# Optimization experiments

Hardware: AMD Instinct MI355X
Metric: run time of the kernel (lower is better)

Reference implementation:

```python
import jax, jax.numpy as jnp
import numpy as np

N, E, G = 100000, 300000, 4096
F_IN, ED, A = 32, 4, 80

def _glorot(k, shape):
    return jax.random.normal(k, shape, dtype=jnp.float32) / np.sqrt(shape[0])

def setup_inputs() -> dict:
    key = jax.random.key(0)
    ks = jax.random.split(key, 24)
    src = jax.random.randint(ks[0], (E,), 0, N, dtype=jnp.int32)
    # guarantee no self loops so PyG's remove_self_loops is a no-op
    dst = ((src + jax.random.randint(ks[1], (E,), 1, N, dtype=jnp.int32)) % N).astype(jnp.int32)
    return dict(
        x=jax.random.normal(ks[2], (N, F_IN), jnp.float32),
        edge_index=jnp.stack([src, dst]),
        edge_attr=jax.random.uniform(ks[3], (E, ED), jnp.float32),
        batch=jnp.sort(jax.random.randint(ks[4], (N,), 0, G, dtype=jnp.int32)),
        action_mask=jnp.ones((G, A), dtype=bool),
        num_graphs=G,
        gin_We=_glorot(ks[5], (ED, F_IN)), gin_be=jnp.zeros((F_IN,), jnp.float32),
        gin_W1=_glorot(ks[6], (F_IN, 64)), gin_b1=jnp.zeros((64,), jnp.float32),
        gin_W2=_glorot(ks[7], (64, 64)), gin_b2=jnp.zeros((64,), jnp.float32),
        g2_Wl=_glorot(ks[8], (64, 256)), g2_bl=jnp.zeros((256,), jnp.float32),
        g2_Wr=_glorot(ks[9], (64, 256)), g2_br=jnp.zeros((256,), jnp.float32),
        g2_We=_glorot(ks[10], (ED, 256)),
        g2_att=jax.random.normal(ks[11], (4, 64), jnp.float32) / np.sqrt(64.0),
        g2_bias=jnp.zeros((256,), jnp.float32),
        g3_Wl=_glorot(ks[12], (256, 256)), g3_bl=jnp.zeros((256,), jnp.float32),
        g3_Wr=_glorot(ks[13], (256, 256)), g3_br=jnp.zeros((256,), jnp.float32),
        g3_We=_glorot(ks[14], (ED, 256)),
        g3_att=jax.random.normal(ks[15], (2, 128), jnp.float32) / np.sqrt(128.0),
        g3_bias=jnp.zeros((128,), jnp.float32),
        pool_W=_glorot(ks[16], (128, 1)), pool_b=jnp.zeros((1,), jnp.float32),
        act_W1=_glorot(ks[17], (128, 64)), act_b1=jnp.zeros((64,), jnp.float32),
        act_W2=_glorot(ks[18], (64, A)), act_b2=jnp.zeros((A,), jnp.float32),
        cr_W1=_glorot(ks[19], (128, 64)), cr_b1=jnp.zeros((64,), jnp.float32),
        cr_W2=_glorot(ks[20], (64, 1)), cr_b2=jnp.zeros((1,), jnp.float32),
    )

def _seg_softmax(s, seg, n):
    # s: [E, H]; softmax over entries sharing seg id (every target has a self loop)
    m = jax.ops.segment_max(s, seg, num_segments=n)
    ex = jnp.exp(s - m[seg])
    z = jax.ops.segment_sum(ex, seg, num_segments=n)
    return ex / z[seg]

def _gatv2(x, src, dst, ea, Wl, bl, Wr, br, We, att, bias, heads, ch, concat, n):
    xl = (x @ Wl + bl).reshape(n, heads, ch)   # message side (x_j)
    xr = (x @ Wr + br).reshape(n, heads, ch)   # target side (x_i)
    e = jax.nn.leaky_relu(xl[src] + xr[dst] + (ea @ We).reshape(-1, heads, ch), 0.2)
    score = jnp.einsum('ehc,hc->eh', e, att)   # [E, H]
    alpha = _seg_softmax(score, dst, n)
    out = jax.ops.segment_sum(xl[src] * alpha[..., None], dst, num_segments=n)
    out = out.reshape(n, heads * ch) if concat else out.mean(axis=1)
    return out + bias

def reference(x, edge_index, edge_attr, batch, action_mask, num_graphs,
              gin_We, gin_be, gin_W1, gin_b1, gin_W2, gin_b2,
              g2_Wl, g2_bl, g2_Wr, g2_br, g2_We, g2_att, g2_bias,
              g3_Wl, g3_bl, g3_Wr, g3_br, g3_We, g3_att, g3_bias,
              pool_W, pool_b, act_W1, act_b1, act_W2, act_b2,
              cr_W1, cr_b1, cr_W2, cr_b2):
    n = x.shape[0]
    src, dst = edge_index[0], edge_index[1]
    # --- GINEConv (eps=0): nn(x + sum_j relu(x_j + lin(e_ij))) ---
    m = jax.nn.relu(x[src] + edge_attr @ gin_We + gin_be)
    h = x + jax.ops.segment_sum(m, dst, num_segments=n)
    h = jax.nn.relu(h @ gin_W1 + gin_b1) @ gin_W2 + gin_b2
    x1 = jax.nn.relu(h)
    # --- self loops with fill_value='mean' edge_attr (shared by both GATv2 layers) ---
    s = jax.ops.segment_sum(edge_attr, dst, num_segments=n)
    cnt = jax.ops.segment_sum(jnp.ones((dst.shape[0],), edge_attr.dtype), dst, num_segments=n)
    loop_attr = s / jnp.maximum(cnt, 1.0)[:, None]
    ar = jnp.arange(n, dtype=src.dtype)
    src2 = jnp.concatenate([src, ar])
    dst2 = jnp.concatenate([dst, ar])
    ea2 = jnp.concatenate([edge_attr, loop_attr], axis=0)
    # --- GATv2 layers ---
    x2 = jax.nn.relu(_gatv2(x1, src2, dst2, ea2, g2_Wl, g2_bl, g2_Wr, g2_br, g2_We, g2_att, g2_bias, 4, 64, True, n))
    x3 = jax.nn.relu(_gatv2(x2, src2, dst2, ea2, g3_Wl, g3_bl, g3_Wr, g3_br, g3_We, g3_att, g3_bias, 2, 128, False, n))
    # --- AttentionalAggregation: softmax(sigmoid(gate), batch) weighted sum ---
    gate = jax.nn.sigmoid(x3 @ pool_W + pool_b)[:, 0]
    alpha = _seg_softmax(gate[:, None], batch, num_graphs)
    emb = jax.ops.segment_sum(alpha * x3, batch, num_segments=num_graphs)
    # --- heads ---
    logits = jax.nn.relu(emb @ act_W1 + act_b1) @ act_W2 + act_b2
    val = jax.nn.relu(emb @ cr_W1 + cr_b1) @ cr_W2 + cr_b2
    logits = jnp.where(action_mask, logits, jnp.finfo(logits.dtype).min)
    return logits, val
```

## Files before the change

### kernel.cpp

```cpp
#include <hip/hip_runtime.h>
#include <math.h>

#define NN 100000
#define NE 300000
#define NG 4096
#define NA 80
#define NB_SCAN 391

typedef __attribute__((ext_vector_type(8))) short short8;
typedef __attribute__((ext_vector_type(4))) float f32x4;

__device__ __forceinline__ float bf2f(unsigned short h){
  return __uint_as_float(((unsigned)h)<<16);
}
__device__ __forceinline__ unsigned short f2bf(float f){
  unsigned u = __float_as_uint(f);
  unsigned r = u + 0x7FFFu + ((u>>16)&1u);
  return (unsigned short)(r>>16);
}
__device__ __forceinline__ void ld_bf4(const unsigned short* p, float o[4]){
  uint2 u = *(const uint2*)p;
  o[0] = __uint_as_float(u.x<<16);
  o[1] = __uint_as_float(u.x & 0xffff0000u);
  o[2] = __uint_as_float(u.y<<16);
  o[3] = __uint_as_float(u.y & 0xffff0000u);
}

__device__ __forceinline__ unsigned fenc(float f){
  unsigned u = __float_as_uint(f);
  return (u & 0x80000000u) ? ~u : (u | 0x80000000u);
}
__device__ __forceinline__ float fdec(unsigned u){
  return (u & 0x80000000u) ? __uint_as_float(u & 0x7fffffffu) : __uint_as_float(~u);
}
#define ENC_NEG_INF 0x007FFFFFu

__global__ __launch_bounds__(256) void fill_u32(unsigned* p, unsigned v, int n){
  int i = blockIdx.x*256 + threadIdx.x;
  if (i < n) p[i] = v;
}

__global__ __launch_bounds__(256) void deg_count(const int* __restrict__ dst, int* __restrict__ deg){
  int e = blockIdx.x*256 + threadIdx.x;
  if (e < NE) atomicAdd(&deg[dst[e]], 1);
}

__global__ __launch_bounds__(256) void scan1(const int* __restrict__ deg, int* __restrict__ row_ptr, int* __restrict__ bsum){
  __shared__ int sh[256];
  int t = threadIdx.x, g = blockIdx.x*256 + t;
  int v = (g < NN) ? deg[g] : 0;
  sh[t] = v;
  __syncthreads();
  for (int off=1; off<256; off<<=1){
    int xv = (t>=off) ? sh[t-off] : 0;
    __syncthreads();
    sh[t] += xv;
    __syncthreads();
  }
  if (g < NN) row_ptr[g] = sh[t] - v;
  if (t == 255) bsum[blockIdx.x] = sh[t];
}

__global__ __launch_bounds__(512) void scan2(int* __restrict__ bsum){
  __shared__ int sh[512];
  int t = threadIdx.x;
  int v = (t < NB_SCAN) ? bsum[t] : 0;
  sh[t] = v;
  __syncthreads();
  for (int off=1; off<512; off<<=1){
    int xv = (t>=off) ? sh[t-off] : 0;
    __syncthreads();
    sh[t] += xv;
    __syncthreads();
  }
  if (t < NB_SCAN) bsum[t] = sh[t] - v;
}

__global__ __launch_bounds__(256) void scan3(int* __restrict__ row_ptr, const int* __restrict__ bsum, int* __restrict__ cursor){
  int g = blockIdx.x*256 + threadIdx.x;
  if (g < NN){
    int r = row_ptr[g] + bsum[g>>8];
    row_ptr[g] = r;
    cursor[g] = r;
  }
}

__global__ __launch_bounds__(256) void scatter_edges(
    const int* __restrict__ dst, const int* __restrict__ src, const float4* __restrict__ ea4,
    int* __restrict__ cursor, int* __restrict__ srcs, float4* __restrict__ eas){
  int e = blockIdx.x*256 + threadIdx.x;
  if (e < NE){
    int pos = atomicAdd(&cursor[dst[e]], 1);
    srcs[pos] = src[e];
    eas[pos]  = ea4[e];
  }
}

__global__ __launch_bounds__(256) void gine_gather(
    const float* __restrict__ x, const int* __restrict__ srcs,
    const int* __restrict__ row_ptr, const int* __restrict__ deg,
    const float4* __restrict__ eas, const float* __restrict__ We, const float* __restrict__ be,
    float* __restrict__ hacc, float* __restrict__ lattr){
  int ch = threadIdx.x & 31, ln = threadIdx.x >> 5;
  int nd = blockIdx.x*8 + ln;
  if (nd >= NN) return;
  int rs = row_ptr[nd], d = deg[nd];
  float accv = 0.f, asum = 0.f;
  float bev = be[ch];
  float w0=We[ch], w1=We[32+ch], w2=We[64+ch], w3=We[96+ch];
  for (int j=0;j<d;++j){
    int s = srcs[rs+j];
    float4 a = eas[rs+j];
    float m = x[s*32+ch] + a.x*w0 + a.y*w1 + a.z*w2 + a.w*w3 + bev;
    accv += (m>0.f)? m : 0.f;
    if (ch < 4) asum += (ch==0)?a.x:(ch==1)?a.y:(ch==2)?a.z:a.w;
  }
  hacc[nd*32+ch] = accv;
  if (ch < 4) lattr[nd*4+ch] = asum / (float)(d>0? d:1);
}

__global__ __launch_bounds__(256) void wt_prep2(
    const float* __restrict__ W, unsigned short* __restrict__ H,
    unsigned short* __restrict__ L, int K, int N){
  int k = blockIdx.x;
  int n = threadIdx.x;
  if (n >= N) return;
  float v = W[k*N + n];
  unsigned short h = f2bf(v);
  unsigned short l = f2bf(v - bf2f(h));
  H[n*K + k] = h;
  L[n*K + k] = l;
}

__global__ __launch_bounds__(512) void gine_mlp_mfma(
    const float* __restrict__ x, const float* __restrict__ hacc,
    const unsigned short* __restrict__ W1h, const unsigned short* __restrict__ W1l,
    const float* __restrict__ b1,
    const unsigned short* __restrict__ W2h, const unsigned short* __restrict__ W2l,
    const float* __restrict__ b2,
    unsigned short* __restrict__ x1b){
  __shared__ unsigned short hS[256*36];
  __shared__ unsigned short t1S[256*68];
  int t = threadIdx.x;
  int row0 = blockIdx.x*256;
  const float4* x4 = (const float4*)x;
  const float4* h4 = (const float4*)hacc;
  #pragma unroll
  for (int j=0;j<4;++j){
    int i = t + j*512;
    int row = i>>3, cq = i&7;
    int grow = row0 + row;
    float4 xv = {0,0,0,0}, hv = {0,0,0,0};
    if (grow < NN){ xv = x4[(size_t)grow*8 + cq]; hv = h4[(size_t)grow*8 + cq]; }
    uint2 o;
    o.x = (unsigned)f2bf(xv.x+hv.x) | ((unsigned)f2bf(xv.y+hv.y)<<16);
    o.y = (unsigned)f2bf(xv.z+hv.z) | ((unsigned)f2bf(xv.w+hv.w)<<16);
    *(uint2*)&hS[row*36 + cq*4] = o;
  }
  int w = t>>6, l = t&63, lr = l&15, lk = l>>4;
  short8 w1h[4], w1l[4];
  #pragma unroll
  for (int nt=0;nt<4;++nt){
    int n = nt*16 + lr;
    w1h[nt] = *(const short8*)(W1h + n*32 + lk*8);
    w1l[nt] = *(const short8*)(W1l + n*32 + lk*8);
  }
  __syncthreads();
  int rw = w*32;
  {
    short8 a0 = *(const short8*)&hS[(rw+lr)*36 + lk*8];
    short8 a1 = *(const short8*)&hS[(rw+16+lr)*36 + lk*8];
    f32x4 acc0[4], acc1[4];
    #pragma unroll
    for (int nt=0;nt<4;++nt){ acc0[nt]=(f32x4){0,0,0,0}; acc1[nt]=(f32x4){0,0,0,0}; }
    #pragma unroll
    for (int nt=0;nt<4;++nt){
      acc0[nt] = __builtin_amdgcn_mfma_f32_16x16x32_bf16(a0, w1h[nt], acc0[nt], 0,0,0);
      acc0[nt] = __builtin_amdgcn_mfma_f32_16x16x32_bf16(a0, w1l[nt], acc0[nt], 0,0,0);
      acc1[nt] = __builtin_amdgcn_mfma_f32_16x16x32_bf16(a1, w1h[nt], acc1[nt], 0,0,0);
      acc1[nt] = __builtin_amdgcn_mfma_f32_16x16x32_bf16(a1, w1l[nt], acc1[nt], 0,0,0);
    }
    #pragma unroll
    for (int nt=0;nt<4;++nt){
      int col = nt*16 + lr;
      float bv = b1[col];
      #pragma unroll
      for (int j=0;j<4;++j){
        int r = rw + lk*4 + j;
        float v0 = acc0[nt][j] + bv; v0 = (v0>0.f)?v0:0.f;
        float v1 = acc1[nt][j] + bv; v1 = (v1>0.f)?v1:0.f;
        t1S[r*68 + col]      = f2bf(v0);
        t1S[(r+16)*68 + col] = f2bf(v1);
      }
    }
  }
  short8 w2h[4][2], w2l[4][2];
  #pragma unroll
  for (int nt=0;nt<4;++nt){
    int n = nt*16 + lr;
    #pragma unroll
    for (int kc=0;kc<2;++kc){
      w2h[nt][kc] = *(const short8*)(W2h + n*64 + kc*32 + lk*8);
      w2l[nt][kc] = *(const short8*)(W2l + n*64 + kc*32 + lk*8);
    }
  }
  __syncthreads();
  {
    f32x4 acc0[4], acc1[4];
    #pragma unroll
    for (int nt=0;nt<4;++nt){ acc0[nt]=(f32x4){0,0,0,0}; acc1[nt]=(f32x4){0,0,0,0}; }
    #pragma unroll
    for (int kc=0;kc<2;++kc){
      short8 a0 = *(const short8*)&t1S[(rw+lr)*68 + kc*32 + lk*8];
      short8 a1 = *(const short8*)&t1S[(rw+16+lr)*68 + kc*32 + lk*8];
      #pragma unroll
      for (int nt=0;nt<4;++nt){
        acc0[nt] = __builtin_amdgcn_mfma_f32_16x16x32_bf16(a0, w2h[nt][kc], acc0[nt], 0,0,0);
        acc0[nt] = __builtin_amdgcn_mfma_f32_16x16x32_bf16(a0, w2l[nt][kc], acc0[nt], 0,0,0);
        acc1[nt] = __builtin_amdgcn_mfma_f32_16x16x32_bf16(a1, w2h[nt][kc], acc1[nt], 0,0,0);
        acc1[nt] = __builtin_amdgcn_mfma_f32_16x16x32_bf16(a1, w2l[nt][kc], acc1[nt], 0,0,0);
      }
    }
    #pragma unroll
    for (int nt=0;nt<4;++nt){
      int col = nt*16 + lr;
      float bv = b2[col];
      #pragma unroll
      for (int j=0;j<4;++j){
        int r0 = row0 + rw + lk*4 + j;
        int r1 = r0 + 16;
        float v0 = acc0[nt][j] + bv; v0 = (v0>0.f)?v0:0.f;
        float v1 = acc1[nt][j] + bv; v1 = (v1>0.f)?v1:0.f;
        if (r0 < NN) x1b[(size_t)r0*64 + col] = f2bf(v0);
        if (r1 < NN) x1b[(size_t)r1*64 + col] = f2bf(v1);
      }
    }
  }
}

template<int KIN>
__global__ __launch_bounds__(512) void mfma_lin(
    const unsigned short* __restrict__ Abf,
    const unsigned short* __restrict__ Wth,
    const unsigned short* __restrict__ Wtl,
    const float* __restrict__ bias,
    unsigned short* __restrict__ Yout){
  __shared__ unsigned short WhS[256*40];
  __shared__ unsigned short WlS[256*40];
  int t = threadIdx.x, w = t>>6, l = t&63;
  int lr = l & 15, lk = l >> 4;
  int row0 = blockIdx.x*256 + w*32;
  f32x4 acc0[16], acc1[16];
  #pragma unroll
  for (int i=0;i<16;++i){ acc0[i] = (f32x4){0,0,0,0}; acc1[i] = (f32x4){0,0,0,0}; }
  int ar0 = row0 + lr;      if (ar0 > NN-1) ar0 = NN-1;
  int ar1 = row0 + 16 + lr; if (ar1 > NN-1) ar1 = NN-1;
  const unsigned short* Ab0 = Abf + (size_t)ar0*KIN + lk*8;
  const unsigned short* Ab1 = Abf + (size_t)ar1*KIN + lk*8;
  const int sn = t>>1, sh16 = (t&1)*16;
  const unsigned short* Wh_g = Wth + (size_t)sn*KIN + sh16;
  const unsigned short* Wl_g = Wtl + (size_t)sn*KIN + sh16;

  short8 ph0, ph1, pl0, pl1;
  ph0 = *(const short8*)(Wh_g);     ph1 = *(const short8*)(Wh_g + 8);
  pl0 = *(const short8*)(Wl_g);     pl1 = *(const short8*)(Wl_g + 8);

  constexpr int NKC = KIN/32;
  for (int kc=0; kc<NKC; ++kc){
    *(short8*)&WhS[sn*40 + sh16]     = ph0;
    *(short8*)&WhS[sn*40 + sh16 + 8] = ph1;
    *(short8*)&WlS[sn*40 + sh16]     = pl0;
    *(short8*)&WlS[sn*40 + sh16 + 8] = pl1;
    __syncthreads();
    if (kc+1 < NKC){
      ph0 = *(const short8*)(Wh_g + (kc+1)*32);
      ph1 = *(const short8*)(Wh_g + (kc+1)*32 + 8);
      pl0 = *(const short8*)(Wl_g + (kc+1)*32);
      pl1 = *(const short8*)(Wl_g + (kc+1)*32 + 8);
    }
    short8 a0 = *(const short8*)(Ab0 + kc*32);
    short8 a1 = *(const short8*)(Ab1 + kc*32);
    #pragma unroll
    for (int nt=0; nt<16; ++nt){
      int n = nt*16 + lr;
      short8 bh = *(const short8*)&WhS[n*40 + lk*8];
      short8 bl = *(const short8*)&WlS[n*40 + lk*8];
      acc0[nt] = __builtin_amdgcn_mfma_f32_16x16x32_bf16(a0, bh, acc0[nt], 0,0,0);
      acc0[nt] = __builtin_amdgcn_mfma_f32_16x16x32_bf16(a0, bl, acc0[nt], 0,0,0);
      acc1[nt] = __builtin_amdgcn_mfma_f32_16x16x32_bf16(a1, bh, acc1[nt], 0,0,0);
      acc1[nt] = __builtin_amdgcn_mfma_f32_16x16x32_bf16(a1, bl, acc1[nt], 0,0,0);
    }
    __syncthreads();
  }

  #pragma unroll
  for (int nt=0; nt<16; ++nt){
    int col = nt*16 + lr;
    float bv = bias[col];
    #pragma unroll
    for (int j=0;j<4;++j){
      int r0 = row0 + lk*4 + j;
      int r1 = r0 + 16;
      if (r0 < NN) Yout[(size_t)r0*256 + col] = f2bf(acc0[nt][j] + bv);
      if (r1 < NN) Yout[(size_t)r1*256 + col] = f2bf(acc1[nt][j] + bv);
    }
  }
}

__global__ __launch_bounds__(256) void gat_fused4(
    const int* __restrict__ srcs, const int* __restrict__ row_ptr,
    const int* __restrict__ deg, const float4* __restrict__ eas,
    const float* __restrict__ lattr,
    const unsigned short* __restrict__ xlb, const unsigned short* __restrict__ xrb,
    const float* __restrict__ We, const float* __restrict__ att,
    const float* __restrict__ bias, unsigned short* __restrict__ x2b){
  int t = threadIdx.x;
  int lane = t & 63, w = t >> 6;
  int nd = blockIdx.x*4 + w;
  if (nd >= NN) return;
  const int c0 = lane*4;
  float4 w0 = *(const float4*)(We + c0);
  float4 w1 = *(const float4*)(We + 256 + c0);
  float4 w2 = *(const float4*)(We + 512 + c0);
  float4 w3 = *(const float4*)(We + 768 + c0);
  float4 at = *(const float4*)(att + c0);
  float4 bs = *(const float4*)(bias + c0);
  float xrv[4]; ld_bf4(xrb + (size_t)nd*256 + c0, xrv);
  float4 la = *(const float4*)(lattr + (size_t)nd*4);
  int rs = row_ptr[nd], d = deg[nd];

  float acc0,acc1,acc2,acc3, m, l;
  {
    float xlv[4]; ld_bf4(xlb + (size_t)nd*256 + c0, xlv);
    float pv, v;
    v = xlv[0]+xrv[0] + la.x*w0.x+la.y*w1.x+la.z*w2.x+la.w*w3.x; v=(v>0.f)?v:0.2f*v; pv  = v*at.x;
    v = xlv[1]+xrv[1] + la.x*w0.y+la.y*w1.y+la.z*w2.y+la.w*w3.y; v=(v>0.f)?v:0.2f*v; pv += v*at.y;
    v = xlv[2]+xrv[2] + la.x*w0.z+la.y*w1.z+la.z*w2.z+la.w*w3.z; v=(v>0.f)?v:0.2f*v; pv += v*at.z;
    v = xlv[3]+xrv[3] + la.x*w0.w+la.y*w1.w+la.z*w2.w+la.w*w3.w; v=(v>0.f)?v:0.2f*v; pv += v*at.w;
    pv += __shfl_xor(pv,1,64); pv += __shfl_xor(pv,2,64);
    pv += __shfl_xor(pv,4,64); pv += __shfl_xor(pv,8,64);
    m = pv; l = 1.f;
    acc0=xlv[0]; acc1=xlv[1]; acc2=xlv[2]; acc3=xlv[3];
  }
  for (int j=0;j<d;++j){
    int s = srcs[rs+j];
    float4 a = eas[rs+j];
    float xlv[4]; ld_bf4(xlb + (size_t)s*256 + c0, xlv);
    float pv, v;
    v = xlv[0]+xrv[0] + a.x*w0.x+a.y*w1.x+a.z*w2.x+a.w*w3.x; v=(v>0.f)?v:0.2f*v; pv  = v*at.x;
    v = xlv[1]+xrv[1] + a.x*w0.y+a.y*w1.y+a.z*w2.y+a.w*w3.y; v=(v>0.f)?v:0.2f*v; pv += v*at.y;
    v = xlv[2]+xrv[2] + a.x*w0.z+a.y*w1.z+a.z*w2.z+a.w*w3.z; v=(v>0.f)?v:0.2f*v; pv += v*at.z;
    v = xlv[3]+xrv[3] + a.x*w0.w+a.y*w1.w+a.z*w2.w+a.w*w3.w; v=(v>0.f)?v:0.2f*v; pv += v*at.w;
    pv += __shfl_xor(pv,1,64); pv += __shfl_xor(pv,2,64);
    pv += __shfl_xor(pv,4,64); pv += __shfl_xor(pv,8,64);
    float mn = fmaxf(m, pv);
    float c1 = __expf(m-mn), c2 = __expf(pv-mn);
    l = l*c1 + c2;
    acc0 = acc0*c1 + c2*xlv[0]; acc1 = acc1*c1 + c2*xlv[1];
    acc2 = acc2*c1 + c2*xlv[2]; acc3 = acc3*c1 + c2*xlv[3];
    m = mn;
  }
  float rl = 1.f/l;
  float o0 = acc0*rl + bs.x; o0 = (o0>0.f)?o0:0.f;
  float o1 = acc1*rl + bs.y; o1 = (o1>0.f)?o1:0.f;
  float o2 = acc2*rl + bs.z; o2 = (o2>0.f)?o2:0.f;
  float o3 = acc3*rl + bs.w; o3 = (o3>0.f)?o3:0.f;
  uint2 ov;
  ov.x = (unsigned)f2bf(o0) | ((unsigned)f2bf(o1)<<16);
  ov.y = (unsigned)f2bf(o2) | ((unsigned)f2bf(o3)<<16);
  *(uint2*)(x2b + (size_t)nd*256 + c0) = ov;
}

__global__ __launch_bounds__(256) void gat_fused2b(
    const int* __restrict__ srcs, const int* __restrict__ row_ptr,
    const int* __restrict__ deg, const float4* __restrict__ eas,
    const float* __restrict__ lattr,
    const unsigned short* __restrict__ xlb, const unsigned short* __restrict__ xrb,
    const float* __restrict__ We, const float* __restrict__ att,
    const float* __restrict__ bias, float* __restrict__ x3){
  int t = threadIdx.x;
  int lane = t & 63, w = t >> 6;
  int nd = blockIdx.x*4 + w;
  if (nd >= NN) return;
  const int c0 = lane*4;
  const int cm = c0 & 127;
  float4 w0 = *(const float4*)(We + c0);
  float4 w1 = *(const float4*)(We + 256 + c0);
  float4 w2 = *(const float4*)(We + 512 + c0);
  float4 w3 = *(const float4*)(We + 768 + c0);
  float4 at = *(const float4*)(att + c0);
  float4 bs = *(const float4*)(bias + cm);
  float xrv[4]; ld_bf4(xrb + (size_t)nd*256 + c0, xrv);
  float4 la = *(const float4*)(lattr + (size_t)nd*4);
  int rs = row_ptr[nd], d = deg[nd];

  float acc0,acc1,acc2,acc3, m, l;
  {
    float xlv[4]; ld_bf4(xlb + (size_t)nd*256 + c0, xlv);
    float pv, v;
    v = xlv[0]+xrv[0] + la.x*w0.x+la.y*w1.x+la.z*w2.x+la.w*w3.x; v=(v>0.f)?v:0.2f*v; pv  = v*at.x;
    v = xlv[1]+xrv[1] + la.x*w0.y+la.y*w1.y+la.z*w2.y+la.w*w3.y; v=(v>0.f)?v:0.2f*v; pv += v*at.y;
    v = xlv[2]+xrv[2] + la.x*w0.z+la.y*w1.z+la.z*w2.z+la.w*w3.z; v=(v>0.f)?v:0.2f*v; pv += v*at.z;
    v = xlv[3]+xrv[3] + la.x*w0.w+la.y*w1.w+la.z*w2.w+la.w*w3.w; v=(v>0.f)?v:0.2f*v; pv += v*at.w;
    pv += __shfl_xor(pv,1,64); pv += __shfl_xor(pv,2,64);
    pv += __shfl_xor(pv,4,64); pv += __shfl_xor(pv,8,64); pv += __shfl_xor(pv,16,64);
    m = pv; l = 1.f;
    acc0=xlv[0]; acc1=xlv[1]; acc2=xlv[2]; acc3=xlv[3];
  }
  for (int j=0;j<d;++j){
    int s = srcs[rs+j];
    float4 a = eas[rs+j];
    float xlv[4]; ld_bf4(xlb + (size_t)s*256 + c0, xlv);
    float pv, v;
    v = xlv[0]+xrv[0] + a.x*w0.x+a.y*w1.x+a.z*w2.x+a.w*w3.x; v=(v>0.f)?v:0.2f*v; pv  = v*at.x;
    v = xlv[1]+xrv[1] + a.x*w0.y+a.y*w1.y+a.z*w2.y+a.w*w3.y; v=(v>0.f)?v:0.2f*v; pv += v*at.y;
    v = xlv[2]+xrv[2] + a.x*w0.z+a.y*w1.z+a.z*w2.z+a.w*w3.z; v=(v>0.f)?v:0.2f*v; pv += v*at.z;
    v = xlv[3]+xrv[3] + a.x*w0.w+a.y*w1.w+a.z*w2.w+a.w*w3.w; v=(v>0.f)?v:0.2f*v; pv += v*at.w;
    pv += __shfl_xor(pv,1,64); pv += __shfl_xor(pv,2,64);
    pv += __shfl_xor(pv,4,64); pv += __shfl_xor(pv,8,64); pv += __shfl_xor(pv,16,64);
    float mn = fmaxf(m, pv);
    float c1 = __expf(m-mn), c2 = __expf(pv-mn);
    l = l*c1 + c2;
    acc0 = acc0*c1 + c2*xlv[0]; acc1 = acc1*c1 + c2*xlv[1];
    acc2 = acc2*c1 + c2*xlv[2]; acc3 = acc3*c1 + c2*xlv[3];
    m = mn;
  }
  float rl = 1.f/l;
  float h0 = acc0*rl, h1 = acc1*rl, h2 = acc2*rl, h3 = acc3*rl;
  float p0 = __shfl_xor(h0,32,64), p1 = __shfl_xor(h1,32,64);
  float p2 = __shfl_xor(h2,32,64), p3 = __shfl_xor(h3,32,64);
  if (lane < 32){
    float4 o;
    o.x = 0.5f*(h0+p0) + bs.x; o.x = (o.x>0.f)?o.x:0.f;
    o.y = 0.5f*(h1+p1) + bs.y; o.y = (o.y>0.f)?o.y:0.f;
    o.z = 0.5f*(h2+p2) + bs.z; o.z = (o.z>0.f)?o.z:0.f;
    o.w = 0.5f*(h3+p3) + bs.w; o.w = (o.w>0.f)?o.w:0.f;
    *(float4*)(x3 + (size_t)nd*128 + c0) = o;
  }
}

__global__ __launch_bounds__(256) void pool_gate(
    const float* __restrict__ x3, const float* __restrict__ pw, const float* __restrict__ pb,
    const int* __restrict__ batch, float* __restrict__ gate, unsigned* __restrict__ gmax){
  int lane = threadIdx.x & 63, le = threadIdx.x >> 6;
  int nd = blockIdx.x*4 + le;
  if (nd >= NN) return;
  float v = x3[nd*128+lane]*pw[lane] + x3[nd*128+64+lane]*pw[64+lane];
  #pragma unroll
  for (int off=32; off; off>>=1) v += __shfl_xor(v, off, 64);
  if (lane == 0){
    float g = 1.f/(1.f + expf(-(v + pb[0])));
    gate[nd] = g;
    atomicMax(&gmax[batch[nd]], fenc(g));
  }
}

__global__ __launch_bounds__(256) void pool_accum(
    const float* __restrict__ x3, const float* __restrict__ gate,
    const unsigned* __restrict__ gmax, const int* __restrict__ batch,
    float* __restrict__ gz, float* __restrict__ emb){
  int lane = threadIdx.x & 63, le = threadIdx.x >> 6;
  int nd = blockIdx.x*4 + le;
  if (nd >= NN) return;
  int b = batch[nd];
  float ex = expf(gate[nd] - fdec(gmax[b]));
  if (lane == 0) unsafeAtomicAdd(&gz[b], ex);
  unsafeAtomicAdd(&emb[b*128+lane],    ex*x3[nd*128+lane]);
  unsafeAtomicAdd(&emb[b*128+64+lane], ex*x3[nd*128+64+lane]);
}

__global__ __launch_bounds__(128) void heads_kernel(
    const float* __restrict__ emb, const float* __restrict__ gz,
    const float* __restrict__ aW1, const float* __restrict__ ab1,
    const float* __restrict__ aW2, const float* __restrict__ ab2,
    const float* __restrict__ cW1, const float* __restrict__ cb1,
    const float* __restrict__ cW2, const float* __restrict__ cb2,
    float* __restrict__ out){
  __shared__ float e[128], t1[64], t2[64];
  int g = blockIdx.x, t = threadIdx.x;
  e[t] = emb[g*128+t] / gz[g];
  __syncthreads();
  if (t < 64){
    float a = ab1[t];
    #pragma unroll 8
    for (int k=0;k<128;++k) a += e[k]*aW1[k*64+t];
    t1[t] = a > 0.f ? a : 0.f;
  } else {
    int j = t - 64;
    float a = cb1[j];
    #pragma unroll 8
    for (int k=0;k<128;++k) a += e[k]*cW1[k*64+j];
    t2[j] = a > 0.f ? a : 0.f;
  }
  __syncthreads();
  if (t < NA){
    float a = ab2[t];
    #pragma unroll 8
    for (int k=0;k<64;++k) a += t1[k]*aW2[k*NA+t];
    out[g*NA+t] = a;
  }
  if (t == 127){
    float a = cb2[0];
    #pragma unroll 8
    for (int k=0;k<64;++k) a += t2[k]*cW2[k];
    out[NG*NA + g] = a;
  }
}

extern "C" void kernel_launch(void* const* d_in, const int* in_sizes, int n_in,
                              void* d_out, int out_size, void* d_ws, size_t ws_size,
                              hipStream_t stream) {
  const float* x      = (const float*)d_in[0];
  const int*   ei     = (const int*)d_in[1];
  const float* eattr  = (const float*)d_in[2];
  const int*   batch  = (const int*)d_in[3];
  const float* gin_We = (const float*)d_in[6];
  const float* gin_be = (const float*)d_in[7];
  const float* gin_W1 = (const float*)d_in[8];
  const float* gin_b1 = (const float*)d_in[9];
  const float* gin_W2 = (const float*)d_in[10];
  const float* gin_b2 = (const float*)d_in[11];
  const float* g2_Wl  = (const float*)d_in[12];
  const float* g2_bl  = (const float*)d_in[13];
  const float* g2_Wr  = (const float*)d_in[14];
  const float* g2_br  = (const float*)d_in[15];
  const float* g2_We  = (const float*)d_in[16];
  const float* g2_att = (const float*)d_in[17];
  const float* g2_bias= (const float*)d_in[18];
  const float* g3_Wl  = (const float*)d_in[19];
  const float* g3_bl  = (const float*)d_in[20];
  const float* g3_Wr  = (const float*)d_in[21];
  const float* g3_br  = (const float*)d_in[22];
  const float* g3_We  = (const float*)d_in[23];
  const float* g3_att = (const float*)d_in[24];
  const float* g3_bias= (const float*)d_in[25];
  const float* pool_W = (const float*)d_in[26];
  const float* pool_b = (const float*)d_in[27];
  const float* act_W1 = (const float*)d_in[28];
  const float* act_b1 = (const float*)d_in[29];
  const float* act_W2 = (const float*)d_in[30];
  const float* act_b2 = (const float*)d_in[31];
  const float* cr_W1  = (const float*)d_in[32];
  const float* cr_b1  = (const float*)d_in[33];
  const float* cr_W2  = (const float*)d_in[34];
  const float* cr_b2  = (const float*)d_in[35];

  const int* src = ei;
  const int* dst = ei + NE;

  char* base = (char*)d_ws;
  size_t off = 0;
  auto take = [&](size_t bytes) -> char* {
    char* p = base + off;
    off += (bytes + 255) & ~(size_t)255;
    return p;
  };
  char* A      = take((size_t)NN*256*4);
  char* B      = take((size_t)NN*256*4);
  unsigned short* x1b = (unsigned short*)take((size_t)NN*64*2);
  float* lattr = (float*)take((size_t)NN*4*4);
  int* deg     = (int*)take((size_t)NN*4);
  int* row_ptr = (int*)take((size_t)NN*4);
  int* cursor  = (int*)take((size_t)NN*4);
  int* srcs    = (int*)take((size_t)NE*4);
  float4* eas  = (float4*)take((size_t)NE*16);
  int* bsum    = (int*)take(512*4);
  float* gate  = (float*)take((size_t)NN*4);
  unsigned* gmax = (unsigned*)take((size_t)NG*4);
  float* gz    = (float*)take((size_t)NG*4);
  float* emb   = (float*)take((size_t)NG*128*4);
  unsigned short* W1h  = (unsigned short*)take(64*32*2);
  unsigned short* W1l  = (unsigned short*)take(64*32*2);
  unsigned short* W2h  = (unsigned short*)take(64*64*2);
  unsigned short* W2l  = (unsigned short*)take(64*64*2);
  unsigned short* W2Lh = (unsigned short*)take(256*64*2);
  unsigned short* W2Ll = (unsigned short*)take(256*64*2);
  unsigned short* W2Rh = (unsigned short*)take(256*64*2);
  unsigned short* W2Rl = (unsigned short*)take(256*64*2);
  unsigned short* W3Lh = (unsigned short*)take(256*256*2);
  unsigned short* W3Ll = (unsigned short*)take(256*256*2);
  unsigned short* W3Rh = (unsigned short*)take(256*256*2);
  unsigned short* W3Rl = (unsigned short*)take(256*256*2);
  if (ws_size < off) return;

  float*          hacc  = (float*)B;
  unsigned short* xl2b  = (unsigned short*)A;
  unsigned short* xr2b  = (unsigned short*)A + (size_t)NN*256;
  unsigned short* x2b   = (unsigned short*)B;
  unsigned short* xl3b  = (unsigned short*)A;
  unsigned short* xr3b  = (unsigned short*)A + (size_t)NN*256;
  float*          x3    = (float*)(B + (size_t)NN*256*2);

  hipMemsetAsync(deg, 0, (size_t)NN*4, stream);
  deg_count<<<(NE+255)/256, 256, 0, stream>>>(dst, deg);
  scan1<<<NB_SCAN, 256, 0, stream>>>(deg, row_ptr, bsum);
  scan2<<<1, 512, 0, stream>>>(bsum);
  scan3<<<NB_SCAN, 256, 0, stream>>>(row_ptr, bsum, cursor);
  scatter_edges<<<(NE+255)/256, 256, 0, stream>>>(dst, src, (const float4*)eattr, cursor, srcs, eas);

  wt_prep2<<<32, 64, 0, stream>>>(gin_W1, W1h, W1l, 32, 64);
  wt_prep2<<<64, 64, 0, stream>>>(gin_W2, W2h, W2l, 64, 64);
  wt_prep2<<<64, 256, 0, stream>>>(g2_Wl, W2Lh, W2Ll, 64, 256);
  wt_prep2<<<64, 256, 0, stream>>>(g2_Wr, W2Rh, W2Rl, 64, 256);
  wt_prep2<<<256, 256, 0, stream>>>(g3_Wl, W3Lh, W3Ll, 256, 256);
  wt_prep2<<<256, 256, 0, stream>>>(g3_Wr, W3Rh, W3Rl, 256, 256);

  gine_gather<<<(NN+7)/8, 256, 0, stream>>>(x, srcs, row_ptr, deg, eas, gin_We, gin_be, hacc, lattr);
  gine_mlp_mfma<<<(NN+255)/256, 512, 0, stream>>>(x, hacc, W1h, W1l, gin_b1, W2h, W2l, gin_b2, x1b);

  const int GEMM_GRID = (NN + 255)/256;

  mfma_lin<64><<<GEMM_GRID, 512, 0, stream>>>(x1b, W2Lh, W2Ll, g2_bl, xl2b);
  mfma_lin<64><<<GEMM_GRID, 512, 0, stream>>>(x1b, W2Rh, W2Rl, g2_br, xr2b);

  gat_fused4<<<(NN+3)/4, 256, 0, stream>>>(srcs, row_ptr, deg, eas, lattr, xl2b, xr2b, g2_We, g2_att, g2_bias, x2b);

  mfma_lin<256><<<GEMM_GRID, 512, 0, stream>>>(x2b, W3Lh, W3Ll, g3_bl, xl3b);
  mfma_lin<256><<<GEMM_GRID, 512, 0, stream>>>(x2b, W3Rh, W3Rl, g3_br, xr3b);

  gat_fused2b<<<(NN+3)/4, 256, 0, stream>>>(srcs, row_ptr, deg, eas, lattr, xl3b, xr3b, g3_We, g3_att, g3_bias, x3);

  fill_u32<<<(NG+255)/256, 256, 0, stream>>>(gmax, ENC_NEG_INF, NG);
  hipMemsetAsync(gz, 0, (size_t)NG*4, stream);
  hipMemsetAsync(emb, 0, (size_t)NG*128*4, stream);
  pool_gate<<<(NN+3)/4, 256, 0, stream>>>(x3, pool_W, pool_b, batch, gate, gmax);
  pool_accum<<<(NN+3)/4, 256, 0, stream>>>(x3, gate, gmax, batch, gz, emb);

  heads_kernel<<<NG, 128, 0, stream>>>(emb, gz, act_W1, act_b1, act_W2, act_b2,
                                       cr_W1, cr_b1, cr_W2, cr_b2, (float*)d_out);
}
```

Baseline: 647.2 us.

## Batch neighbor gathers, prefetch GEMM A tiles, fuse pooling and weight prep

The GINE gather and both GATv2 aggregation loops now process neighbors in groups of four. Their loads are issued together, and the online softmax is updated once per group, so memory latency overlaps across edges. The MFMA linear kernel prefetches the next A fragment alongside the weight prefetch. The six weight-split launches become one kernel. Pooling drops the per-graph max pass, since the sigmoid gate is bounded in (0,1), which fuses gate and accumulate into one kernel. The cost is more registers per thread and one fewer launch-ordering pass.

```diff
diff --git a/kernel.cpp b/kernel.cpp
--- a/kernel.cpp
+++ b/kernel.cpp
@@ -24,20 +24,6 @@
   o[1] = __uint_as_float(u.x & 0xffff0000u);
   o[2] = __uint_as_float(u.y<<16);
   o[3] = __uint_as_float(u.y & 0xffff0000u);
-}
-
-__device__ __forceinline__ unsigned fenc(float f){
-  unsigned u = __float_as_uint(f);
-  return (u & 0x80000000u) ? ~u : (u | 0x80000000u);
-}
-__device__ __forceinline__ float fdec(unsigned u){
-  return (u & 0x80000000u) ? __uint_as_float(u & 0x7fffffffu) : __uint_as_float(~u);
-}
-#define ENC_NEG_INF 0x007FFFFFu
-
-__global__ __launch_bounds__(256) void fill_u32(unsigned* p, unsigned v, int n){
-  int i = blockIdx.x*256 + threadIdx.x;
-  if (i < n) p[i] = v;
 }
 
 __global__ __launch_bounds__(256) void deg_count(const int* __restrict__ dst, int* __restrict__ deg){
@@ -108,22 +94,49 @@
   float accv = 0.f, asum = 0.f;
   float bev = be[ch];
   float w0=We[ch], w1=We[32+ch], w2=We[64+ch], w3=We[96+ch];
-  for (int j=0;j<d;++j){
-    int s = srcs[rs+j];
-    float4 a = eas[rs+j];
-    float m = x[s*32+ch] + a.x*w0 + a.y*w1 + a.z*w2 + a.w*w3 + bev;
-    accv += (m>0.f)? m : 0.f;
-    if (ch < 4) asum += (ch==0)?a.x:(ch==1)?a.y:(ch==2)?a.z:a.w;
+  for (int j0=0; j0<d; j0+=4){
+    int sv[4]; float4 av[4];
+    #pragma unroll
+    for (int i=0;i<4;++i){
+      int jj = j0+i;
+      if (jj < d){ sv[i]=srcs[rs+jj]; av[i]=eas[rs+jj]; }
+      else { sv[i]=-1; av[i]=(float4){0,0,0,0}; }
+    }
+    float xv[4];
+    #pragma unroll
+    for (int i=0;i<4;++i) xv[i] = (sv[i]>=0) ? x[(size_t)sv[i]*32+ch] : 0.f;
+    #pragma unroll
+    for (int i=0;i<4;++i){
+      if (sv[i]>=0){
+        float4 a = av[i];
+        float mm = xv[i] + a.x*w0 + a.y*w1 + a.z*w2 + a.w*w3 + bev;
+        accv += (mm>0.f)? mm : 0.f;
+        if (ch < 4) asum += (ch==0)?a.x:(ch==1)?a.y:(ch==2)?a.z:a.w;
+      }
+    }
   }
   hacc[nd*32+ch] = accv;
   if (ch < 4) lattr[nd*4+ch] = asum / (float)(d>0? d:1);
 }
 
-__global__ __launch_bounds__(256) void wt_prep2(
-    const float* __restrict__ W, unsigned short* __restrict__ H,
-    unsigned short* __restrict__ L, int K, int N){
-  int k = blockIdx.x;
-  int n = threadIdx.x;
+__global__ __launch_bounds__(256) void wt_prep_all(
+    const float* __restrict__ gW1, const float* __restrict__ gW2,
+    const float* __restrict__ g2Wl, const float* __restrict__ g2Wr,
+    const float* __restrict__ g3Wl, const float* __restrict__ g3Wr,
+    unsigned short* __restrict__ W1h, unsigned short* __restrict__ W1l,
+    unsigned short* __restrict__ W2h, unsigned short* __restrict__ W2l,
+    unsigned short* __restrict__ W2Lh, unsigned short* __restrict__ W2Ll,
+    unsigned short* __restrict__ W2Rh, unsigned short* __restrict__ W2Rl,
+    unsigned short* __restrict__ W3Lh, unsigned short* __restrict__ W3Ll,
+    unsigned short* __restrict__ W3Rh, unsigned short* __restrict__ W3Rl){
+  int b = blockIdx.x, n = threadIdx.x;
+  const float* W; unsigned short *H, *L; int K, N, k;
+  if (b < 32)      { W=gW1;  H=W1h;  L=W1l;  K=32;  N=64;  k=b; }
+  else if (b < 96) { W=gW2;  H=W2h;  L=W2l;  K=64;  N=64;  k=b-32; }
+  else if (b < 160){ W=g2Wl; H=W2Lh; L=W2Ll; K=64;  N=256; k=b-96; }
+  else if (b < 224){ W=g2Wr; H=W2Rh; L=W2Rl; K=64;  N=256; k=b-160; }
+  else if (b < 480){ W=g3Wl; H=W3Lh; L=W3Ll; K=256; N=256; k=b-224; }
+  else             { W=g3Wr; H=W3Rh; L=W3Rl; K=256; N=256; k=b-480; }
   if (n >= N) return;
   float v = W[k*N + n];
   unsigned short h = f2bf(v);
@@ -264,6 +277,8 @@
   short8 ph0, ph1, pl0, pl1;
   ph0 = *(const short8*)(Wh_g);     ph1 = *(const short8*)(Wh_g + 8);
   pl0 = *(const short8*)(Wl_g);     pl1 = *(const short8*)(Wl_g + 8);
+  short8 a0 = *(const short8*)(Ab0);
+  short8 a1 = *(const short8*)(Ab1);
 
   constexpr int NKC = KIN/32;
   for (int kc=0; kc<NKC; ++kc){
@@ -272,14 +287,15 @@
     *(short8*)&WlS[sn*40 + sh16]     = pl0;
     *(short8*)&WlS[sn*40 + sh16 + 8] = pl1;
     __syncthreads();
+    short8 na0, na1;
     if (kc+1 < NKC){
       ph0 = *(const short8*)(Wh_g + (kc+1)*32);
       ph1 = *(const short8*)(Wh_g + (kc+1)*32 + 8);
       pl0 = *(const short8*)(Wl_g + (kc+1)*32);
       pl1 = *(const short8*)(Wl_g + (kc+1)*32 + 8);
-    }
-    short8 a0 = *(const short8*)(Ab0 + kc*32);
-    short8 a1 = *(const short8*)(Ab1 + kc*32);
+      na0 = *(const short8*)(Ab0 + (kc+1)*32);
+      na1 = *(const short8*)(Ab1 + (kc+1)*32);
+    }
     #pragma unroll
     for (int nt=0; nt<16; ++nt){
       int n = nt*16 + lr;
@@ -290,6 +306,7 @@
       acc1[nt] = __builtin_amdgcn_mfma_f32_16x16x32_bf16(a1, bh, acc1[nt], 0,0,0);
       acc1[nt] = __builtin_amdgcn_mfma_f32_16x16x32_bf16(a1, bl, acc1[nt], 0,0,0);
     }
+    if (kc+1 < NKC){ a0 = na0; a1 = na1; }
     __syncthreads();
   }
 
@@ -329,35 +346,53 @@
   float4 la = *(const float4*)(lattr + (size_t)nd*4);
   int rs = row_ptr[nd], d = deg[nd];
 
-  float acc0,acc1,acc2,acc3, m, l;
-  {
-    float xlv[4]; ld_bf4(xlb + (size_t)nd*256 + c0, xlv);
-    float pv, v;
-    v = xlv[0]+xrv[0] + la.x*w0.x+la.y*w1.x+la.z*w2.x+la.w*w3.x; v=(v>0.f)?v:0.2f*v; pv  = v*at.x;
-    v = xlv[1]+xrv[1] + la.x*w0.y+la.y*w1.y+la.z*w2.y+la.w*w3.y; v=(v>0.f)?v:0.2f*v; pv += v*at.y;
-    v = xlv[2]+xrv[2] + la.x*w0.z+la.y*w1.z+la.z*w2.z+la.w*w3.z; v=(v>0.f)?v:0.2f*v; pv += v*at.z;
-    v = xlv[3]+xrv[3] + la.x*w0.w+la.y*w1.w+la.z*w2.w+la.w*w3.w; v=(v>0.f)?v:0.2f*v; pv += v*at.w;
-    pv += __shfl_xor(pv,1,64); pv += __shfl_xor(pv,2,64);
-    pv += __shfl_xor(pv,4,64); pv += __shfl_xor(pv,8,64);
-    m = pv; l = 1.f;
-    acc0=xlv[0]; acc1=xlv[1]; acc2=xlv[2]; acc3=xlv[3];
-  }
-  for (int j=0;j<d;++j){
-    int s = srcs[rs+j];
-    float4 a = eas[rs+j];
-    float xlv[4]; ld_bf4(xlb + (size_t)s*256 + c0, xlv);
-    float pv, v;
-    v = xlv[0]+xrv[0] + a.x*w0.x+a.y*w1.x+a.z*w2.x+a.w*w3.x; v=(v>0.f)?v:0.2f*v; pv  = v*at.x;
-    v = xlv[1]+xrv[1] + a.x*w0.y+a.y*w1.y+a.z*w2.y+a.w*w3.y; v=(v>0.f)?v:0.2f*v; pv += v*at.y;
-    v = xlv[2]+xrv[2] + a.x*w0.z+a.y*w1.z+a.z*w2.z+a.w*w3.z; v=(v>0.f)?v:0.2f*v; pv += v*at.z;
-    v = xlv[3]+xrv[3] + a.x*w0.w+a.y*w1.w+a.z*w2.w+a.w*w3.w; v=(v>0.f)?v:0.2f*v; pv += v*at.w;
-    pv += __shfl_xor(pv,1,64); pv += __shfl_xor(pv,2,64);
-    pv += __shfl_xor(pv,4,64); pv += __shfl_xor(pv,8,64);
-    float mn = fmaxf(m, pv);
-    float c1 = __expf(m-mn), c2 = __expf(pv-mn);
-    l = l*c1 + c2;
-    acc0 = acc0*c1 + c2*xlv[0]; acc1 = acc1*c1 + c2*xlv[1];
-    acc2 = acc2*c1 + c2*xlv[2]; acc3 = acc3*c1 + c2*xlv[3];
+  float acc0=0.f, acc1=0.f, acc2=0.f, acc3=0.f;
+  float m = -3.0e38f, l = 0.f;
+  for (int j0=-1; j0<d; j0+=4){
+    int sv[4]; float4 ev[4];
+    #pragma unroll
+    for (int i=0;i<4;++i){
+      int jj = j0+i;
+      if (jj < 0){ sv[i]=nd; ev[i]=la; }
+      else if (jj < d){ sv[i]=srcs[rs+jj]; ev[i]=eas[rs+jj]; }
+      else { sv[i]=-1; ev[i]=(float4){0,0,0,0}; }
+    }
+    float xs[4][4];
+    #pragma unroll
+    for (int i=0;i<4;++i){
+      if (sv[i] >= 0) ld_bf4(xlb + (size_t)sv[i]*256 + c0, xs[i]);
+      else { xs[i][0]=0.f; xs[i][1]=0.f; xs[i][2]=0.f; xs[i][3]=0.f; }
+    }
+    float p[4];
+    #pragma unroll
+    for (int i=0;i<4;++i){
+      float4 a = ev[i];
+      float v, pv;
+      v = xs[i][0]+xrv[0] + a.x*w0.x+a.y*w1.x+a.z*w2.x+a.w*w3.x; v=(v>0.f)?v:0.2f*v; pv  = v*at.x;
+      v = xs[i][1]+xrv[1] + a.x*w0.y+a.y*w1.y+a.z*w2.y+a.w*w3.y; v=(v>0.f)?v:0.2f*v; pv += v*at.y;
+      v = xs[i][2]+xrv[2] + a.x*w0.z+a.y*w1.z+a.z*w2.z+a.w*w3.z; v=(v>0.f)?v:0.2f*v; pv += v*at.z;
+      v = xs[i][3]+xrv[3] + a.x*w0.w+a.y*w1.w+a.z*w2.w+a.w*w3.w; v=(v>0.f)?v:0.2f*v; pv += v*at.w;
+      p[i] = pv;
+    }
+    #pragma unroll
+    for (int st=1; st<=8; st<<=1){
+      p[0] += __shfl_xor(p[0],st,64);
+      p[1] += __shfl_xor(p[1],st,64);
+      p[2] += __shfl_xor(p[2],st,64);
+      p[3] += __shfl_xor(p[3],st,64);
+    }
+    #pragma unroll
+    for (int i=0;i<4;++i) if (sv[i] < 0) p[i] = -3.0e38f;
+    float mx = fmaxf(fmaxf(p[0],p[1]), fmaxf(p[2],p[3]));
+    float mn = fmaxf(m, mx);
+    float c  = __expf(m-mn);
+    float e0 = __expf(p[0]-mn), e1 = __expf(p[1]-mn);
+    float e2 = __expf(p[2]-mn), e3 = __expf(p[3]-mn);
+    l = l*c + e0+e1+e2+e3;
+    acc0 = acc0*c + e0*xs[0][0] + e1*xs[1][0] + e2*xs[2][0] + e3*xs[3][0];
+    acc1 = acc1*c + e0*xs[0][1] + e1*xs[1][1] + e2*xs[2][1] + e3*xs[3][1];
+    acc2 = acc2*c + e0*xs[0][2] + e1*xs[1][2] + e2*xs[2][2] + e3*xs[3][2];
+    acc3 = acc3*c + e0*xs[0][3] + e1*xs[1][3] + e2*xs[2][3] + e3*xs[3][3];
     m = mn;
   }
   float rl = 1.f/l;
@@ -394,35 +429,53 @@
   float4 la = *(const float4*)(lattr + (size_t)nd*4);
   int rs = row_ptr[nd], d = deg[nd];
 
-  float acc0,acc1,acc2,acc3, m, l;
-  {
-    float xlv[4]; ld_bf4(xlb + (size_t)nd*256 + c0, xlv);
-    float pv, v;
-    v = xlv[0]+xrv[0] + la.x*w0.x+la.y*w1.x+la.z*w2.x+la.w*w3.x; v=(v>0.f)?v:0.2f*v; pv  = v*at.x;
-    v = xlv[1]+xrv[1] + la.x*w0.y+la.y*w1.y+la.z*w2.y+la.w*w3.y; v=(v>0.f)?v:0.2f*v; pv += v*at.y;
-    v = xlv[2]+xrv[2] + la.x*w0.z+la.y*w1.z+la.z*w2.z+la.w*w3.z; v=(v>0.f)?v:0.2f*v; pv += v*at.z;
-    v = xlv[3]+xrv[3] + la.x*w0.w+la.y*w1.w+la.z*w2.w+la.w*w3.w; v=(v>0.f)?v:0.2f*v; pv += v*at.w;
-    pv += __shfl_xor(pv,1,64); pv += __shfl_xor(pv,2,64);
-    pv += __shfl_xor(pv,4,64); pv += __shfl_xor(pv,8,64); pv += __shfl_xor(pv,16,64);
-    m = pv; l = 1.f;
-    acc0=xlv[0]; acc1=xlv[1]; acc2=xlv[2]; acc3=xlv[3];
-  }
-  for (int j=0;j<d;++j){
-    int s = srcs[rs+j];
-    float4 a = eas[rs+j];
-    float xlv[4]; ld_bf4(xlb + (size_t)s*256 + c0, xlv);
-    float pv, v;
-    v = xlv[0]+xrv[0] + a.x*w0.x+a.y*w1.x+a.z*w2.x+a.w*w3.x; v=(v>0.f)?v:0.2f*v; pv  = v*at.x;
-    v = xlv[1]+xrv[1] + a.x*w0.y+a.y*w1.y+a.z*w2.y+a.w*w3.y; v=(v>0.f)?v:0.2f*v; pv += v*at.y;
-    v = xlv[2]+xrv[2] + a.x*w0.z+a.y*w1.z+a.z*w2.z+a.w*w3.z; v=(v>0.f)?v:0.2f*v; pv += v*at.z;
-    v = xlv[3]+xrv[3] + a.x*w0.w+a.y*w1.w+a.z*w2.w+a.w*w3.w; v=(v>0.f)?v:0.2f*v; pv += v*at.w;
-    pv += __shfl_xor(pv,1,64); pv += __shfl_xor(pv,2,64);
-    pv += __shfl_xor(pv,4,64); pv += __shfl_xor(pv,8,64); pv += __shfl_xor(pv,16,64);
-    float mn = fmaxf(m, pv);
-    float c1 = __expf(m-mn), c2 = __expf(pv-mn);
-    l = l*c1 + c2;
-    acc0 = acc0*c1 + c2*xlv[0]; acc1 = acc1*c1 + c2*xlv[1];
-    acc2 = acc2*c1 + c2*xlv[2]; acc3 = acc3*c1 + c2*xlv[3];
+  float acc0=0.f, acc1=0.f, acc2=0.f, acc3=0.f;
+  float m = -3.0e38f, l = 0.f;
+  for (int j0=-1; j0<d; j0+=4){
+    int sv[4]; float4 ev[4];
+    #pragma unroll
+    for (int i=0;i<4;++i){
+      int jj = j0+i;
+      if (jj < 0){ sv[i]=nd; ev[i]=la; }
+      else if (jj < d){ sv[i]=srcs[rs+jj]; ev[i]=eas[rs+jj]; }
+      else { sv[i]=-1; ev[i]=(float4){0,0,0,0}; }
+    }
+    float xs[4][4];
+    #pragma unroll
+    for (int i=0;i<4;++i){
+      if (sv[i] >= 0) ld_bf4(xlb + (size_t)sv[i]*256 + c0, xs[i]);
+      else { xs[i][0]=0.f; xs[i][1]=0.f; xs[i][2]=0.f; xs[i][3]=0.f; }
+    }
+    float p[4];
+    #pragma unroll
+    for (int i=0;i<4;++i){
+      float4 a = ev[i];
+      float v, pv;
+      v = xs[i][0]+xrv[0] + a.x*w0.x+a.y*w1.x+a.z*w2.x+a.w*w3.x; v=(v>0.f)?v:0.2f*v; pv  = v*at.x;
+      v = xs[i][1]+xrv[1] + a.x*w0.y+a.y*w1.y+a.z*w2.y+a.w*w3.y; v=(v>0.f)?v:0.2f*v; pv += v*at.y;
+      v = xs[i][2]+xrv[2] + a.x*w0.z+a.y*w1.z+a.z*w2.z+a.w*w3.z; v=(v>0.f)?v:0.2f*v; pv += v*at.z;
+      v = xs[i][3]+xrv[3] + a.x*w0.w+a.y*w1.w+a.z*w2.w+a.w*w3.w; v=(v>0.f)?v:0.2f*v; pv += v*at.w;
+      p[i] = pv;
+    }
+    #pragma unroll
+    for (int st=1; st<=16; st<<=1){
+      p[0] += __shfl_xor(p[0],st,64);
+      p[1] += __shfl_xor(p[1],st,64);
+      p[2] += __shfl_xor(p[2],st,64);
+      p[3] += __shfl_xor(p[3],st,64);
+    }
+    #pragma unroll
+    for (int i=0;i<4;++i) if (sv[i] < 0) p[i] = -3.0e38f;
+    float mx = fmaxf(fmaxf(p[0],p[1]), fmaxf(p[2],p[3]));
+    float mn = fmaxf(m, mx);
+    float c  = __expf(m-mn);
+    float e0 = __expf(p[0]-mn), e1 = __expf(p[1]-mn);
+    float e2 = __expf(p[2]-mn), e3 = __expf(p[3]-mn);
+    l = l*c + e0+e1+e2+e3;
+    acc0 = acc0*c + e0*xs[0][0] + e1*xs[1][0] + e2*xs[2][0] + e3*xs[3][0];
+    acc1 = acc1*c + e0*xs[0][1] + e1*xs[1][1] + e2*xs[2][1] + e3*xs[3][1];
+    acc2 = acc2*c + e0*xs[0][2] + e1*xs[1][2] + e2*xs[2][2] + e3*xs[3][2];
+    acc3 = acc3*c + e0*xs[0][3] + e1*xs[1][3] + e2*xs[2][3] + e3*xs[3][3];
     m = mn;
   }
   float rl = 1.f/l;
@@ -439,34 +492,29 @@
   }
 }
 
-__global__ __launch_bounds__(256) void pool_gate(
+__global__ __launch_bounds__(256) void pool_init(float* __restrict__ gz, float* __restrict__ emb){
+  int i = blockIdx.x*256 + threadIdx.x;
+  if (i < NG) gz[i] = 0.f;
+  if (i < NG*128) emb[i] = 0.f;
+}
+
+__global__ __launch_bounds__(256) void pool_fused(
     const float* __restrict__ x3, const float* __restrict__ pw, const float* __restrict__ pb,
-    const int* __restrict__ batch, float* __restrict__ gate, unsigned* __restrict__ gmax){
+    const int* __restrict__ batch, float* __restrict__ gz, float* __restrict__ emb){
   int lane = threadIdx.x & 63, le = threadIdx.x >> 6;
   int nd = blockIdx.x*4 + le;
   if (nd >= NN) return;
-  float v = x3[nd*128+lane]*pw[lane] + x3[nd*128+64+lane]*pw[64+lane];
+  float v0 = x3[(size_t)nd*128+lane];
+  float v1 = x3[(size_t)nd*128+64+lane];
+  float v = v0*pw[lane] + v1*pw[64+lane];
   #pragma unroll
   for (int off=32; off; off>>=1) v += __shfl_xor(v, off, 64);
-  if (lane == 0){
-    float g = 1.f/(1.f + expf(-(v + pb[0])));
-    gate[nd] = g;
-    atomicMax(&gmax[batch[nd]], fenc(g));
-  }
-}
-
-__global__ __launch_bounds__(256) void pool_accum(
-    const float* __restrict__ x3, const float* __restrict__ gate,
-    const unsigned* __restrict__ gmax, const int* __restrict__ batch,
-    float* __restrict__ gz, float* __restrict__ emb){
-  int lane = threadIdx.x & 63, le = threadIdx.x >> 6;
-  int nd = blockIdx.x*4 + le;
-  if (nd >= NN) return;
+  float g = 1.f/(1.f + expf(-(v + pb[0])));
+  float ex = expf(g);
   int b = batch[nd];
-  float ex = expf(gate[nd] - fdec(gmax[b]));
   if (lane == 0) unsafeAtomicAdd(&gz[b], ex);
-  unsafeAtomicAdd(&emb[b*128+lane],    ex*x3[nd*128+lane]);
-  unsafeAtomicAdd(&emb[b*128+64+lane], ex*x3[nd*128+64+lane]);
+  unsafeAtomicAdd(&emb[b*128+lane],    ex*v0);
+  unsafeAtomicAdd(&emb[b*128+64+lane], ex*v1);
 }
 
 __global__ __launch_bounds__(128) void heads_kernel(
@@ -565,8 +613,6 @@
   int* srcs    = (int*)take((size_t)NE*4);
   float4* eas  = (float4*)take((size_t)NE*16);
   int* bsum    = (int*)take(512*4);
-  float* gate  = (float*)take((size_t)NN*4);
-  unsigned* gmax = (unsigned*)take((size_t)NG*4);
   float* gz    = (float*)take((size_t)NG*4);
   float* emb   = (float*)take((size_t)NG*128*4);
   unsigned short* W1h  = (unsigned short*)take(64*32*2);
@@ -598,12 +644,9 @@
   scan3<<<NB_SCAN, 256, 0, stream>>>(row_ptr, bsum, cursor);
   scatter_edges<<<(NE+255)/256, 256, 0, stream>>>(dst, src, (const float4*)eattr, cursor, srcs, eas);
 
-  wt_prep2<<<32, 64, 0, stream>>>(gin_W1, W1h, W1l, 32, 64);
-  wt_prep2<<<64, 64, 0, stream>>>(gin_W2, W2h, W2l, 64, 64);
-  wt_prep2<<<64, 256, 0, stream>>>(g2_Wl, W2Lh, W2Ll, 64, 256);
-  wt_prep2<<<64, 256, 0, stream>>>(g2_Wr, W2Rh, W2Rl, 64, 256);
-  wt_prep2<<<256, 256, 0, stream>>>(g3_Wl, W3Lh, W3Ll, 256, 256);
-  wt_prep2<<<256, 256, 0, stream>>>(g3_Wr, W3Rh, W3Rl, 256, 256);
+  wt_prep_all<<<736, 256, 0, stream>>>(gin_W1, gin_W2, g2_Wl, g2_Wr, g3_Wl, g3_Wr,
+                                       W1h, W1l, W2h, W2l, W2Lh, W2Ll, W2Rh, W2Rl,
+                                       W3Lh, W3Ll, W3Rh, W3Rl);
 
   gine_gather<<<(NN+7)/8, 256, 0, stream>>>(x, srcs, row_ptr, deg, eas, gin_We, gin_be, hacc, lattr);
   gine_mlp_mfma<<<(NN+255)/256, 512, 0, stream>>>(x, hacc, W1h, W1l, gin_b1, W2h, W2l, gin_b2, x1b);
@@ -620,11 +663,8 @@
 
   gat_fused2b<<<(NN+3)/4, 256, 0, stream>>>(srcs, row_ptr, deg, eas, lattr, xl3b, xr3b, g3_We, g3_att, g3_bias, x3);
 
-  fill_u32<<<(NG+255)/256, 256, 0, stream>>>(gmax, ENC_NEG_INF, NG);
-  hipMemsetAsync(gz, 0, (size_t)NG*4, stream);
-  hipMemsetAsync(emb, 0, (size_t)NG*128*4, stream);
-  pool_gate<<<(NN+3)/4, 256, 0, stream>>>(x3, pool_W, pool_b, batch, gate, gmax);
-  pool_accum<<<(NN+3)/4, 256, 0, stream>>>(x3, gate, gmax, batch, gz, emb);
+  pool_init<<<(NG*128+255)/256, 256, 0, stream>>>(gz, emb);
+  pool_fused<<<(NN+3)/4, 256, 0, stream>>>(x3, pool_W, pool_b, batch, gz, emb);
 
   heads_kernel<<<NG, 128, 0, stream>>>(emb, gz, act_W1, act_b1, act_W2, act_b2,
                                        cr_W1, cr_b1, cr_W2, cr_b2, (float*)d_out);
```

After: 708.9 us. +9.5%, slower.
